# Kernel tuning notes

Hardware: AMD Instinct MI355X
Metric: run time of the kernel (lower is better)

## Reference

```python
import jax, jax.numpy as jnp
import numpy as np

N, P, D, C = 8192, 512, 2, 4   # queries, coeff grid points, spatial dim, num coefficients
HA = 32                        # attention_net hidden
HP, CP = 32, 16                # pointswise_mlp hidden / output
HG = 256                       # green_function_net hidden


def setup_inputs() -> dict:
    key = jax.random.key(0)
    ks = jax.random.split(key, 16)
    g = lambda k, shp, s: jax.random.normal(k, shp, dtype=jnp.float32) * s
    return {
        "r": g(ks[0], (N, 2 * D), 1.0),
        "r_prime": g(ks[1], (N, 2 * D), 1.0),
        "coeff_x": g(ks[2], (P, D), 1.0),
        "coeff_y": g(ks[3], (P, C), 1.0),
        # attention_net MLP (no bias): concat(q,k)=4 -> 32 -> 32 -> 1
        "Wa1": g(ks[4], (2 * D, HA), 0.5),
        "Wa2": g(ks[5], (HA, HA), 1.0 / np.sqrt(HA)),
        "Wa3": g(ks[6], (HA, 1), 1.0 / np.sqrt(HA)),
        # pointswise_mlp: C -> 32 -> 16
        "Wp1": g(ks[7], (C, HP), 0.5), "bp1": jnp.zeros((HP,), jnp.float32),
        "Wp2": g(ks[8], (HP, CP), 1.0 / np.sqrt(HP)), "bp2": jnp.zeros((CP,), jnp.float32),
        # green_function_net: 4+4+16=24 -> 256 -> 256 -> 1 (exp at the end)
        "Wg1": g(ks[9], (2 * D + 2 * D + CP, HG), 1.0 / np.sqrt(24.0)), "bg1": jnp.zeros((HG,), jnp.float32),
        "Wg2": g(ks[10], (HG, HG), 1.0 / np.sqrt(HG)), "bg2": jnp.zeros((HG,), jnp.float32),
        "Wg3": g(ks[11], (HG, 1), 0.1 / np.sqrt(HG)), "bg3": jnp.zeros((1,), jnp.float32),
    }


def reference(r, r_prime, coeff_x, coeff_y,
              Wa1, Wa2, Wa3, Wp1, bp1, Wp2, bp2,
              Wg1, bg1, Wg2, bg2, Wg3, bg3):
    # --- CoefficientNet: pairwise MLP attention over the coefficient grid ---
    q = r[:, :D]  # (N, 2) spatial position only
    # first layer of attn MLP on concat([q, k]) split into q- and k- parts
    h = jax.nn.relu(q @ Wa1[:D][None if False else slice(None)]  # (N, HA)
                    [..., :] [..., :]  # no-op for readability
                    if False else (q @ Wa1[:D])[:, None, :] + (coeff_x @ Wa1[D:])[None, :, :])  # (N, P, HA)
    h = jax.nn.relu(h @ Wa2)                     # (N, P, HA)
    logits = (h @ Wa3)[..., 0]                   # (N, P)
    attn = jax.nn.softmax(logits, axis=-1)       # (N, P)
    attn_out = attn @ coeff_y                    # (N, C)
    c = jax.nn.relu(attn_out @ Wp1 + bp1) @ Wp2 + bp2  # (N, CP)
    # --- GreenFunctionNet ---
    x = jnp.concatenate([r, r_prime, c], axis=-1)       # (N, 24)
    g1 = jax.nn.relu(x @ Wg1 + bg1)
    g2 = jax.nn.relu(g1 @ Wg2 + bg2)
    return jnp.exp(g2 @ Wg3 + bg3)                      # (N, 1)
```

## Files before the change

### kernel.cpp

```cpp
#include <hip/hip_runtime.h>
#include <math.h>

#define N_ 8192
#define P_ 512

typedef __fp16 half8  __attribute__((ext_vector_type(8)));
typedef __fp16 half2t __attribute__((ext_vector_type(2)));
typedef float  floatx16 __attribute__((ext_vector_type(16)));

union H8 { half8 v; half2t h2[4]; };

static __device__ __forceinline__ half2t pk2(float a, float b) {
    return __builtin_amdgcn_cvt_pkrtz(a, b);
}

__global__ __launch_bounds__(512, 2) void k_attn(
    const float* __restrict__ r,
    const float* __restrict__ coeff_x,
    const float* __restrict__ coeff_y,
    const float* __restrict__ Wa1,
    const float* __restrict__ Wa2,
    const float* __restrict__ Wa3,
    float* __restrict__ ws_s,
    float* __restrict__ ws_ao)
{
    __shared__ __align__(16) unsigned char bpS[256 * 96];
    __shared__ __align__(16) float4 cyS[256];
    __shared__ float sA[8][32];
    __shared__ float aoA[4][8][32];

    const int tid    = threadIdx.x;
    const int ntile  = blockIdx.x >> 1;
    const int pblock = (blockIdx.x & 1) * 256;
    const int n0     = ntile * 32;
    const int lane   = tid & 63;
    const int wv     = tid >> 6;
    const int j32    = lane & 31;
    const int hl     = lane >> 5;
    const int k0g    = hl * 8;

    if (tid < 256) {
        const float2 cx = ((const float2*)coeff_x)[pblock + tid];
        half2t* wrow = (half2t*)(bpS + tid * 96);
#pragma unroll
        for (int q = 0; q < 16; ++q) {
            const float b0 = cx.x * Wa1[64 + 2*q]     + cx.y * Wa1[96 + 2*q];
            const float b1 = cx.x * Wa1[64 + 2*q + 1] + cx.y * Wa1[96 + 2*q + 1];
            wrow[q] = pk2(b0, b1);
        }
    } else {
        cyS[tid - 256] = ((const float4*)coeff_y)[pblock + tid - 256];
    }

    half2t anh1[4], anh2[4];
    {
        const float2 rv = ((const float2*)r)[2 * (n0 + j32)];
#pragma unroll
        for (int q = 0; q < 4; ++q) {
            const int k1 = k0g + 2*q, k2 = 16 + k0g + 2*q;
            anh1[q] = pk2(rv.x*Wa1[k1]   + rv.y*Wa1[32+k1],
                          rv.x*Wa1[k1+1] + rv.y*Wa1[32+k1+1]);
            anh2[q] = pk2(rv.x*Wa1[k2]   + rv.y*Wa1[32+k2],
                          rv.x*Wa1[k2+1] + rv.y*Wa1[32+k2+1]);
        }
    }
    H8 af1, af2;
#pragma unroll
    for (int q = 0; q < 4; ++q) {
        af1.h2[q] = pk2(Wa2[(k0g + 2*q)     * 32 + j32],
                        Wa2[(k0g + 2*q + 1) * 32 + j32]);
        af2.h2[q] = pk2(Wa2[(16 + k0g + 2*q)     * 32 + j32],
                        Wa2[(16 + k0g + 2*q + 1) * 32 + j32]);
    }
    half2t w3h[8];
#pragma unroll
    for (int q = 0; q < 8; ++q) {
        const int r0 = ((2*q) & 3) + 8*(q >> 1) + 4*hl;
        w3h[q] = pk2(Wa3[r0], Wa3[r0 + 1]);
    }

    __syncthreads();

    const half2t zero2 = pk2(0.f, 0.f);
    float s = 0.0f, aox = 0.f, aoy = 0.f, aoz = 0.f, aow = 0.f;

#pragma unroll 2
    for (int pl = 0; pl < 32; ++pl) {
        const int ploc = wv * 32 + pl;
        const half2t* rowq = (const half2t*)(bpS + ploc * 96) + hl * 4;

        H8 bf1, bf2;
#pragma unroll
        for (int q = 0; q < 4; ++q) {
            bf1.h2[q] = __builtin_elementwise_max(anh1[q] + rowq[q],     zero2);
            bf2.h2[q] = __builtin_elementwise_max(anh2[q] + rowq[8 + q], zero2);
        }

        floatx16 zc = {};
        floatx16 acc = __builtin_amdgcn_mfma_f32_32x32x16_f16(af1.v, bf1.v, zc, 0, 0, 0);
        acc = __builtin_amdgcn_mfma_f32_32x32x16_f16(af2.v, bf2.v, acc, 0, 0, 0);

        float d0 = 0.f, d1 = 0.f;
#pragma unroll
        for (int q = 0; q < 8; q += 2) {
            half2t z0 = __builtin_elementwise_max(pk2(acc[2*q],   acc[2*q+1]), zero2);
            half2t z1 = __builtin_elementwise_max(pk2(acc[2*q+2], acc[2*q+3]), zero2);
            d0 = __builtin_amdgcn_fdot2(z0, w3h[q],   d0, false);
            d1 = __builtin_amdgcn_fdot2(z1, w3h[q+1], d1, false);
        }
        float dot = d0 + d1;
        dot += __shfl_xor(dot, 32);

        const float e = __expf(dot);
        const float4 cyv = cyS[ploc];
        s   += e;
        aox += e * cyv.x;
        aoy += e * cyv.y;
        aoz += e * cyv.z;
        aow += e * cyv.w;
    }

    if (lane < 32) {
        sA[wv][lane]      = s;
        aoA[0][wv][lane]  = aox;
        aoA[1][wv][lane]  = aoy;
        aoA[2][wv][lane]  = aoz;
        aoA[3][wv][lane]  = aow;
    }
    __syncthreads();

    if (tid < 32) {
        float S = 0.f, A0 = 0.f, A1 = 0.f, A2 = 0.f, A3 = 0.f;
#pragma unroll
        for (int w = 0; w < 8; ++w) {
            S  += sA[w][tid];
            A0 += aoA[0][w][tid];
            A1 += aoA[1][w][tid];
            A2 += aoA[2][w][tid];
            A3 += aoA[3][w][tid];
        }
        const int n = n0 + tid;
        atomicAdd(ws_s + n, S);
        atomicAdd(ws_ao + n*4 + 0, A0);
        atomicAdd(ws_ao + n*4 + 1, A1);
        atomicAdd(ws_ao + n*4 + 2, A2);
        atomicAdd(ws_ao + n*4 + 3, A3);
    }
}

#define HP_OFF 17408
#define XS_OFF 21760

__global__ __launch_bounds__(512) void k_rest(
    const float* __restrict__ r,
    const float* __restrict__ rp,
    const float* __restrict__ ws_s,
    const float* __restrict__ ws_ao,
    const float* __restrict__ Wp1,
    const float* __restrict__ bp1,
    const float* __restrict__ Wp2,
    const float* __restrict__ bp2,
    const float* __restrict__ Wg1,
    const float* __restrict__ bg1,
    const float* __restrict__ Wg2,
    const float* __restrict__ bg2,
    const float* __restrict__ Wg3,
    const float* __restrict__ bg3,
    float* __restrict__ out)
{
    __shared__ __align__(16) unsigned char reg0[25984];
    __shared__ float redS[8][32];
    __shared__ float aoS[32][4];

    const int tid  = threadIdx.x;
    const int n0   = blockIdx.x * 32;
    const int lane = tid & 63;
    const int wv   = tid >> 6;
    const int j32  = lane & 31;
    const int hl   = lane >> 5;
    const int k0g  = hl * 8;

    float* hpS = (float*)(reg0 + HP_OFF);
    float* xS  = (float*)(reg0 + XS_OFF);
    const int nB = tid & 31;
    const int iB = tid >> 5;

    if (tid < 32) {
        const float inv = 1.0f / ws_s[n0 + tid];
#pragma unroll
        for (int c = 0; c < 4; ++c)
            aoS[tid][c] = ws_ao[(n0 + tid)*4 + c] * inv;
    }
    if (tid < 256) {
        const int nn = tid >> 3, k = tid & 7;
        xS[nn*25 + k] = (k < 4) ? r[(n0+nn)*4 + k] : rp[(n0+nn)*4 + k - 4];
    }
    __syncthreads();

    {
        const float a0 = aoS[nB][0], a1 = aoS[nB][1], a2 = aoS[nB][2], a3 = aoS[nB][3];
#pragma unroll
        for (int rep = 0; rep < 2; ++rep) {
            const int i = iB + rep*16;
            float a = bp1[i] + a0*Wp1[i] + a1*Wp1[32+i] + a2*Wp1[64+i] + a3*Wp1[96+i];
            hpS[nB*33 + i] = fmaxf(a, 0.0f);
        }
    }
    __syncthreads();

    {
        float a = bp2[iB];
#pragma unroll
        for (int i = 0; i < 32; ++i) a += hpS[nB*33 + i] * Wp2[i*16 + iB];
        xS[nB*25 + 8 + iB] = a;
    }
    __syncthreads();

    const int jcol = (wv << 5) + j32;
    __fp16* g1S = (__fp16*)reg0;
    {
        H8 xa1, xa2, wb1, wb2;
        const float* xrow = xS + j32 * 25;
#pragma unroll
        for (int q = 0; q < 4; ++q) {
            xa1.h2[q] = pk2(xrow[k0g + 2*q], xrow[k0g + 2*q + 1]);
            wb1.h2[q] = pk2(Wg1[(k0g + 2*q)*256 + jcol],
                            Wg1[(k0g + 2*q + 1)*256 + jcol]);
            if (hl == 0) {
                xa2.h2[q] = pk2(xrow[16 + 2*q], xrow[16 + 2*q + 1]);
                wb2.h2[q] = pk2(Wg1[(16 + 2*q)*256 + jcol],
                                Wg1[(17 + 2*q)*256 + jcol]);
            } else {
                xa2.h2[q] = pk2(0.f, 0.f);
                wb2.h2[q] = pk2(0.f, 0.f);
            }
        }
        floatx16 g1acc = {};
        g1acc = __builtin_amdgcn_mfma_f32_32x32x16_f16(xa1.v, wb1.v, g1acc, 0, 0, 0);
        g1acc = __builtin_amdgcn_mfma_f32_32x32x16_f16(xa2.v, wb2.v, g1acc, 0, 0, 0);

        const float b1v = bg1[jcol];
#pragma unroll
        for (int i = 0; i < 16; ++i) {
            const int row = (i & 3) + 8*(i >> 2) + 4*hl;
            g1S[row*264 + jcol] = (__fp16)fmaxf(g1acc[i] + b1v, 0.0f);
        }
    }
    __syncthreads();

    {
        H8 wB[16];
#pragma unroll
        for (int kk = 0; kk < 16; ++kk) {
            const int kb = kk*16 + hl*8;
#pragma unroll
            for (int q = 0; q < 4; ++q)
                wB[kk].h2[q] = pk2(Wg2[(kb + 2*q)*256 + jcol],
                                   Wg2[(kb + 2*q + 1)*256 + jcol]);
        }
        floatx16 acc2 = {};
        const __fp16* arow = g1S + j32 * 264;
#pragma unroll
        for (int kk = 0; kk < 16; ++kk) {
            H8 af;
            af.v = *(const half8*)(arow + kk*16 + hl*8);
            acc2 = __builtin_amdgcn_mfma_f32_32x32x16_f16(af.v, wB[kk].v, acc2, 0, 0, 0);
        }

        const float b2v = bg2[jcol];
        const float w3v = Wg3[jcol];
        float part[16];
#pragma unroll
        for (int i = 0; i < 16; ++i)
            part[i] = fmaxf(acc2[i] + b2v, 0.0f) * w3v;
#pragma unroll
        for (int off = 1; off <= 16; off <<= 1) {
#pragma unroll
            for (int i = 0; i < 16; ++i) part[i] += __shfl_xor(part[i], off);
        }
        if ((lane & 31) == 0) {
#pragma unroll
            for (int i = 0; i < 16; ++i) {
                const int row = (i & 3) + 8*(i >> 2) + 4*hl;
                redS[wv][row] = part[i];
            }
        }
        __syncthreads();

        if (tid < 32) {
            float v = bg3[0];
#pragma unroll
            for (int w = 0; w < 8; ++w) v += redS[w][tid];
            out[n0 + tid] = __expf(v);
        }
    }
}

extern "C" void kernel_launch(void* const* d_in, const int* in_sizes, int n_in,
                              void* d_out, int out_size, void* d_ws, size_t ws_size,
                              hipStream_t stream)
{
    const float* r   = (const float*)d_in[0];
    const float* rp  = (const float*)d_in[1];
    const float* cx  = (const float*)d_in[2];
    const float* cy  = (const float*)d_in[3];
    const float* Wa1 = (const float*)d_in[4];
    const float* Wa2 = (const float*)d_in[5];
    const float* Wa3 = (const float*)d_in[6];
    const float* Wp1 = (const float*)d_in[7];
    const float* bp1 = (const float*)d_in[8];
    const float* Wp2 = (const float*)d_in[9];
    const float* bp2 = (const float*)d_in[10];
    const float* Wg1 = (const float*)d_in[11];
    const float* bg1 = (const float*)d_in[12];
    const float* Wg2 = (const float*)d_in[13];
    const float* bg2 = (const float*)d_in[14];
    const float* Wg3 = (const float*)d_in[15];
    const float* bg3 = (const float*)d_in[16];

    float* ws_s  = (float*)d_ws;
    float* ws_ao = ws_s + N_;

    (void)hipMemsetAsync(d_ws, 0, (size_t)N_ * 5 * sizeof(float), stream);

    hipLaunchKernelGGL(k_attn, dim3(512),   dim3(512), 0, stream,
                       r, cx, cy, Wa1, Wa2, Wa3, ws_s, ws_ao);
    hipLaunchKernelGGL(k_rest, dim3(N_/32), dim3(512), 0, stream,
                       r, rp, ws_s, ws_ao, Wp1, bp1, Wp2, bp2,
                       Wg1, bg1, Wg2, bg2, Wg3, bg3, (float*)d_out);
}
```

Measured before the change: 113.7 us.

## Split attention into smaller blocks and software-prefetch LDS rows per iteration

Each block of the attention kernel now covers 128 coefficient points with 256 threads instead of 256 points with 512 threads, so the grid grows to 1024 blocks with four partial blocks per query tile. The inner loop reads the next row of the first-layer bias and the next coeff_y value from LDS one iteration ahead, as vectorized half8 loads, to hide LDS latency behind the MFMAs. The final dot product is split into four independent accumulation chains for more instruction-level parallelism. The price is twice as many global atomics per query, a smaller block for hiding latency, and extra registers for the prefetch buffers.

```diff
diff --git a/kernel.cpp b/kernel.cpp
--- a/kernel.cpp
+++ b/kernel.cpp
@@ -14,7 +14,7 @@
     return __builtin_amdgcn_cvt_pkrtz(a, b);
 }
 
-__global__ __launch_bounds__(512, 2) void k_attn(
+__global__ __launch_bounds__(256, 4) void k_attn(
     const float* __restrict__ r,
     const float* __restrict__ coeff_x,
     const float* __restrict__ coeff_y,
@@ -24,14 +24,14 @@
     float* __restrict__ ws_s,
     float* __restrict__ ws_ao)
 {
-    __shared__ __align__(16) unsigned char bpS[256 * 96];
-    __shared__ __align__(16) float4 cyS[256];
-    __shared__ float sA[8][32];
-    __shared__ float aoA[4][8][32];
+    __shared__ __align__(16) unsigned char bpS[128 * 96];
+    __shared__ __align__(16) float4 cyS[128];
+    __shared__ float sA[4][32];
+    __shared__ float aoA[4][4][32];
 
     const int tid    = threadIdx.x;
-    const int ntile  = blockIdx.x >> 1;
-    const int pblock = (blockIdx.x & 1) * 256;
+    const int ntile  = blockIdx.x >> 2;
+    const int pblock = (blockIdx.x & 3) * 128;
     const int n0     = ntile * 32;
     const int lane   = tid & 63;
     const int wv     = tid >> 6;
@@ -39,7 +39,7 @@
     const int hl     = lane >> 5;
     const int k0g    = hl * 8;
 
-    if (tid < 256) {
+    if (tid < 128) {
         const float2 cx = ((const float2*)coeff_x)[pblock + tid];
         half2t* wrow = (half2t*)(bpS + tid * 96);
 #pragma unroll
@@ -49,19 +49,19 @@
             wrow[q] = pk2(b0, b1);
         }
     } else {
-        cyS[tid - 256] = ((const float4*)coeff_y)[pblock + tid - 256];
-    }
-
-    half2t anh1[4], anh2[4];
+        cyS[tid - 128] = ((const float4*)coeff_y)[pblock + tid - 128];
+    }
+
+    H8 anh1, anh2;
     {
         const float2 rv = ((const float2*)r)[2 * (n0 + j32)];
 #pragma unroll
         for (int q = 0; q < 4; ++q) {
             const int k1 = k0g + 2*q, k2 = 16 + k0g + 2*q;
-            anh1[q] = pk2(rv.x*Wa1[k1]   + rv.y*Wa1[32+k1],
-                          rv.x*Wa1[k1+1] + rv.y*Wa1[32+k1+1]);
-            anh2[q] = pk2(rv.x*Wa1[k2]   + rv.y*Wa1[32+k2],
-                          rv.x*Wa1[k2+1] + rv.y*Wa1[32+k2+1]);
+            anh1.h2[q] = pk2(rv.x*Wa1[k1]   + rv.y*Wa1[32+k1],
+                             rv.x*Wa1[k1+1] + rv.y*Wa1[32+k1+1]);
+            anh2.h2[q] = pk2(rv.x*Wa1[k2]   + rv.y*Wa1[32+k2],
+                             rv.x*Wa1[k2+1] + rv.y*Wa1[32+k2+1]);
         }
     }
     H8 af1, af2;
@@ -84,40 +84,60 @@
     const half2t zero2 = pk2(0.f, 0.f);
     float s = 0.0f, aox = 0.f, aoy = 0.f, aoz = 0.f, aow = 0.f;
 
+    const unsigned char* base = bpS + (wv * 32) * 96 + hl * 16;
+
+    H8 c0, c1;  float4 cyv;
+    c0.v = *(const half8*)(base);
+    c1.v = *(const half8*)(base + 32);
+    cyv  = cyS[wv * 32];
+
 #pragma unroll 2
     for (int pl = 0; pl < 32; ++pl) {
-        const int ploc = wv * 32 + pl;
-        const half2t* rowq = (const half2t*)(bpS + ploc * 96) + hl * 4;
+        H8 nx0, nx1;  float4 cyn;
+        if (pl < 31) {
+            const unsigned char* nb = base + (pl + 1) * 96;
+            nx0.v = *(const half8*)(nb);
+            nx1.v = *(const half8*)(nb + 32);
+            cyn   = cyS[wv * 32 + pl + 1];
+        }
 
         H8 bf1, bf2;
 #pragma unroll
         for (int q = 0; q < 4; ++q) {
-            bf1.h2[q] = __builtin_elementwise_max(anh1[q] + rowq[q],     zero2);
-            bf2.h2[q] = __builtin_elementwise_max(anh2[q] + rowq[8 + q], zero2);
+            bf1.h2[q] = __builtin_elementwise_max(anh1.h2[q] + c0.h2[q], zero2);
+            bf2.h2[q] = __builtin_elementwise_max(anh2.h2[q] + c1.h2[q], zero2);
         }
 
         floatx16 zc = {};
         floatx16 acc = __builtin_amdgcn_mfma_f32_32x32x16_f16(af1.v, bf1.v, zc, 0, 0, 0);
         acc = __builtin_amdgcn_mfma_f32_32x32x16_f16(af2.v, bf2.v, acc, 0, 0, 0);
 
-        float d0 = 0.f, d1 = 0.f;
-#pragma unroll
-        for (int q = 0; q < 8; q += 2) {
-            half2t z0 = __builtin_elementwise_max(pk2(acc[2*q],   acc[2*q+1]), zero2);
-            half2t z1 = __builtin_elementwise_max(pk2(acc[2*q+2], acc[2*q+3]), zero2);
-            d0 = __builtin_amdgcn_fdot2(z0, w3h[q],   d0, false);
-            d1 = __builtin_amdgcn_fdot2(z1, w3h[q+1], d1, false);
-        }
-        float dot = d0 + d1;
+        float d0, d1, d2, d3;
+        {
+            half2t z0 = __builtin_elementwise_max(pk2(acc[0],  acc[1]),  zero2);
+            half2t z1 = __builtin_elementwise_max(pk2(acc[2],  acc[3]),  zero2);
+            half2t z2 = __builtin_elementwise_max(pk2(acc[4],  acc[5]),  zero2);
+            half2t z3 = __builtin_elementwise_max(pk2(acc[6],  acc[7]),  zero2);
+            half2t z4 = __builtin_elementwise_max(pk2(acc[8],  acc[9]),  zero2);
+            half2t z5 = __builtin_elementwise_max(pk2(acc[10], acc[11]), zero2);
+            half2t z6 = __builtin_elementwise_max(pk2(acc[12], acc[13]), zero2);
+            half2t z7 = __builtin_elementwise_max(pk2(acc[14], acc[15]), zero2);
+            d0 = __builtin_amdgcn_fdot2(z1, w3h[1], __builtin_amdgcn_fdot2(z0, w3h[0], 0.f, false), false);
+            d1 = __builtin_amdgcn_fdot2(z3, w3h[3], __builtin_amdgcn_fdot2(z2, w3h[2], 0.f, false), false);
+            d2 = __builtin_amdgcn_fdot2(z5, w3h[5], __builtin_amdgcn_fdot2(z4, w3h[4], 0.f, false), false);
+            d3 = __builtin_amdgcn_fdot2(z7, w3h[7], __builtin_amdgcn_fdot2(z6, w3h[6], 0.f, false), false);
+        }
+        float dot = (d0 + d1) + (d2 + d3);
         dot += __shfl_xor(dot, 32);
 
         const float e = __expf(dot);
-        const float4 cyv = cyS[ploc];
         s   += e;
         aox += e * cyv.x;
         aoy += e * cyv.y;
         aoz += e * cyv.z;
         aow += e * cyv.w;
+
+        c0 = nx0; c1 = nx1; cyv = cyn;
     }
 
     if (lane < 32) {
@@ -132,7 +152,7 @@
     if (tid < 32) {
         float S = 0.f, A0 = 0.f, A1 = 0.f, A2 = 0.f, A3 = 0.f;
 #pragma unroll
-        for (int w = 0; w < 8; ++w) {
+        for (int w = 0; w < 4; ++w) {
             S  += sA[w][tid];
             A0 += aoA[0][w][tid];
             A1 += aoA[1][w][tid];
@@ -323,7 +343,7 @@
 
     (void)hipMemsetAsync(d_ws, 0, (size_t)N_ * 5 * sizeof(float), stream);
 
-    hipLaunchKernelGGL(k_attn, dim3(512),   dim3(512), 0, stream,
+    hipLaunchKernelGGL(k_attn, dim3(1024),  dim3(256), 0, stream,
                        r, cx, cy, Wa1, Wa2, Wa3, ws_s, ws_ao);
     hipLaunchKernelGGL(k_rest, dim3(N_/32), dim3(512), 0, stream,
                        r, rp, ws_s, ws_ao, Wp1, bp1, Wp2, bp2,
```

Result: no change. 115.9 us (+1.9%).
